# Kernel tuning notes

Measured on AMD Instinct MI355X. Metric: run time of the kernel, lower is better.

Reference implementation:

```python
import jax, jax.numpy as jnp
import numpy as np

EPS = 1e-5

def setup_inputs() -> dict:
    key = jax.random.key(0)
    k1, k2, k3, k4, k5 = jax.random.split(key, 5)
    B, C, H, W = 4, 256, 256, 256  # W == C == input_features (LayerNorm over last dim)
    O = 256  # output_features
    x = jax.random.normal(k1, (B, C, H, W), dtype=jnp.float32)
    y = jax.random.normal(k2, (B, C, H, W), dtype=jnp.float32)
    ln_weight = jax.random.normal(k3, (W,), dtype=jnp.float32) * 0.02 + 1.0
    ln_bias = jax.random.normal(k4, (W,), dtype=jnp.float32) * 0.02
    conv_weight = jax.random.normal(k5, (O, C), dtype=jnp.float32) * (1.0 / np.sqrt(C))  # 1x1 conv, no bias
    return {"x": x, "y": y, "ln_weight": ln_weight, "ln_bias": ln_bias, "conv_weight": conv_weight}


def reference(x, y, ln_weight, ln_bias, conv_weight):
    # residual add
    out = x + y  # [B, C, H, W]
    # LayerNorm over the last dim (W), matching nn.LayerNorm(normalized_shape=input_features)
    mean = jnp.mean(out, axis=-1, keepdims=True)
    var = jnp.mean(jnp.square(out - mean), axis=-1, keepdims=True)
    normed = (out - mean) * jax.lax.rsqrt(var + EPS) * ln_weight + ln_bias
    # 1x1 Conv2d (per-pixel matmul over channels), bias=False
    conv = jnp.einsum("bchw,oc->bohw", normed, conv_weight)
    # ReLU
    return jnp.maximum(conv, 0.0)
```

## Files before the change

### kernel.cpp

```cpp
#include <hip/hip_runtime.h>

typedef __bf16 bf16x8 __attribute__((ext_vector_type(8)));
typedef float floatx4 __attribute__((ext_vector_type(4)));

__device__ __forceinline__ unsigned short f2bf(float f) {
    unsigned int u = __builtin_bit_cast(unsigned int, f);
    u += 0x7fffu + ((u >> 16) & 1u);
    return (unsigned short)(u >> 16);
}

__global__ __launch_bounds__(256) void prep_kernel(const float* __restrict__ cw,
                                                   unsigned short* __restrict__ cwb,
                                                   float* __restrict__ S) {
    int o = blockIdx.x;
    int c = threadIdx.x;
    float w = cw[o * 256 + c];
    cwb[o * 256 + c] = f2bf(w);
    float s = w;
    #pragma unroll
    for (int off = 32; off; off >>= 1) s += __shfl_xor(s, off);
    __shared__ float ps[4];
    if ((c & 63) == 0) ps[c >> 6] = s;
    __syncthreads();
    if (c == 0) S[o] = ps[0] + ps[1] + ps[2] + ps[3];
}

__global__ __launch_bounds__(256) void ln_kernel(const float* __restrict__ x,
                                                 const float* __restrict__ y,
                                                 const float* __restrict__ lnw,
                                                 unsigned short* __restrict__ zhat) {
    int wave = threadIdx.x >> 6;
    int lane = threadIdx.x & 63;
    size_t row = (size_t)blockIdx.x * 4 + wave;
    const float4* xp = (const float4*)(x + row * 256) + lane;
    const float4* yp = (const float4*)(y + row * 256) + lane;
    float4 xv = *xp;
    float4 yv = *yp;
    float z0 = xv.x + yv.x, z1 = xv.y + yv.y, z2 = xv.z + yv.z, z3 = xv.w + yv.w;
    float s = z0 + z1 + z2 + z3;
    float q = z0 * z0 + z1 * z1 + z2 * z2 + z3 * z3;
    #pragma unroll
    for (int off = 32; off; off >>= 1) {
        s += __shfl_xor(s, off);
        q += __shfl_xor(q, off);
    }
    float mean = s * (1.0f / 256.0f);
    float var = q * (1.0f / 256.0f) - mean * mean;
    float rstd = rsqrtf(var + 1e-5f);
    float4 w4 = *((const float4*)lnw + lane);
    ushort4 ov;
    ov.x = f2bf((z0 - mean) * rstd * w4.x);
    ov.y = f2bf((z1 - mean) * rstd * w4.y);
    ov.z = f2bf((z2 - mean) * rstd * w4.z);
    ov.w = f2bf((z3 - mean) * rstd * w4.w);
    *((ushort4*)(zhat + row * 256) + lane) = ov;
}

__global__ __launch_bounds__(256) void gemm_kernel(const unsigned short* __restrict__ zhat,
                                                   const unsigned short* __restrict__ cwb,
                                                   const float* __restrict__ S,
                                                   const float* __restrict__ lnb,
                                                   float* __restrict__ out) {
    constexpr int LDK = 264;
    __shared__ unsigned short bt[64 * LDK];

    int id = blockIdx.x;
    int b = id >> 10;
    int tile = id & 1023;
    int p0 = tile * 64;
    const unsigned short* zb = zhat + ((size_t)b << 24) + p0;
    int t = threadIdx.x;

    {
        int c0 = t >> 3;
        int n0 = (t & 7) * 8;
        #pragma unroll
        for (int pass = 0; pass < 8; ++pass) {
            int c = c0 + pass * 32;
            uint4 v = *(const uint4*)(zb + (size_t)c * 65536 + n0);
            unsigned int vv[4] = {v.x, v.y, v.z, v.w};
            #pragma unroll
            for (int q = 0; q < 4; ++q) {
                bt[(n0 + 2 * q + 0) * LDK + c] = (unsigned short)(vv[q] & 0xffffu);
                bt[(n0 + 2 * q + 1) * LDK + c] = (unsigned short)(vv[q] >> 16);
            }
        }
    }
    __syncthreads();

    int wave = t >> 6;
    int lane = t & 63;
    int llo = lane & 15;
    int lhi = lane >> 4;
    int o_base = wave * 64;

    floatx4 acc[4][4];
    #pragma unroll
    for (int u = 0; u < 4; ++u)
        #pragma unroll
        for (int s = 0; s < 4; ++s)
            #pragma unroll
            for (int r = 0; r < 4; ++r) acc[u][s][r] = 0.0f;

    #pragma unroll
    for (int kt = 0; kt < 8; ++kt) {
        int k0 = kt * 32;
        bf16x8 bfrag[4], afrag[4];
        #pragma unroll
        for (int s = 0; s < 4; ++s)
            bfrag[s] = *(const bf16x8*)&bt[(16 * s + llo) * LDK + k0 + lhi * 8];
        #pragma unroll
        for (int u = 0; u < 4; ++u)
            afrag[u] = *(const bf16x8*)(cwb + (size_t)(o_base + 16 * u + llo) * 256 + k0 + lhi * 8);
        #pragma unroll
        for (int u = 0; u < 4; ++u)
            #pragma unroll
            for (int s = 0; s < 4; ++s)
                acc[u][s] = __builtin_amdgcn_mfma_f32_16x16x32_bf16(afrag[u], bfrag[s], acc[u][s], 0, 0, 0);
    }

    float lnbv[4];
    #pragma unroll
    for (int s = 0; s < 4; ++s) lnbv[s] = lnb[(p0 + 16 * s + llo) & 255];
    float* outb = out + ((size_t)b << 24) + p0;
    #pragma unroll
    for (int u = 0; u < 4; ++u) {
        #pragma unroll
        for (int r = 0; r < 4; ++r) {
            int o = o_base + 16 * u + 4 * lhi + r;
            float so = S[o];
            #pragma unroll
            for (int s = 0; s < 4; ++s) {
                float v = acc[u][s][r] + so * lnbv[s];
                v = v > 0.0f ? v : 0.0f;
                outb[(size_t)o * 65536 + 16 * s + llo] = v;
            }
        }
    }
}

extern "C" void kernel_launch(void* const* d_in, const int* in_sizes, int n_in,
                              void* d_out, int out_size, void* d_ws, size_t ws_size,
                              hipStream_t stream) {
    const float* x   = (const float*)d_in[0];
    const float* y   = (const float*)d_in[1];
    const float* lnw = (const float*)d_in[2];
    const float* lnb = (const float*)d_in[3];
    const float* cw  = (const float*)d_in[4];
    float* out = (float*)d_out;

    unsigned short* zhat = (unsigned short*)d_ws;
    unsigned short* cwb  = (unsigned short*)((char*)d_ws + (size_t)134217728);
    float* S             = (float*)((char*)d_ws + (size_t)134217728 + 131072);

    prep_kernel<<<256, 256, 0, stream>>>(cw, cwb, S);
    ln_kernel<<<65536, 256, 0, stream>>>(x, y, lnw, zhat);
    gemm_kernel<<<4096, 256, 0, stream>>>(zhat, cwb, S, lnb, out);
}
```

Before: 691.2 us.

## Fuse residual LayerNorm into 1x1-conv GEMM via LDS-staged bf16 tile per row

```diff
diff --git a/kernel.cpp b/kernel.cpp
--- a/kernel.cpp
+++ b/kernel.cpp
@@ -25,115 +25,122 @@
     if (c == 0) S[o] = ps[0] + ps[1] + ps[2] + ps[3];
 }
 
-__global__ __launch_bounds__(256) void ln_kernel(const float* __restrict__ x,
-                                                 const float* __restrict__ y,
-                                                 const float* __restrict__ lnw,
-                                                 unsigned short* __restrict__ zhat) {
-    int wave = threadIdx.x >> 6;
-    int lane = threadIdx.x & 63;
-    size_t row = (size_t)blockIdx.x * 4 + wave;
-    const float4* xp = (const float4*)(x + row * 256) + lane;
-    const float4* yp = (const float4*)(y + row * 256) + lane;
-    float4 xv = *xp;
-    float4 yv = *yp;
-    float z0 = xv.x + yv.x, z1 = xv.y + yv.y, z2 = xv.z + yv.z, z3 = xv.w + yv.w;
-    float s = z0 + z1 + z2 + z3;
-    float q = z0 * z0 + z1 * z1 + z2 * z2 + z3 * z3;
+__global__ __launch_bounds__(512) void fused_kernel(const float* __restrict__ x,
+                                                    const float* __restrict__ y,
+                                                    const float* __restrict__ lnw,
+                                                    const float* __restrict__ lnb,
+                                                    const unsigned short* __restrict__ cwb,
+                                                    const float* __restrict__ S,
+                                                    float* __restrict__ out) {
+    __shared__ unsigned short zt[256 * 256];
+
+    int b = blockIdx.x >> 8;
+    int h = blockIdx.x & 255;
+    int t = threadIdx.x;
+    int wave = t >> 6;
+    int lane = t & 63;
+    size_t plane = ((size_t)b << 24) + ((size_t)h << 8);
+
+    float lw[4];
     #pragma unroll
-    for (int off = 32; off; off >>= 1) {
-        s += __shfl_xor(s, off);
-        q += __shfl_xor(q, off);
-    }
-    float mean = s * (1.0f / 256.0f);
-    float var = q * (1.0f / 256.0f) - mean * mean;
-    float rstd = rsqrtf(var + 1e-5f);
-    float4 w4 = *((const float4*)lnw + lane);
-    ushort4 ov;
-    ov.x = f2bf((z0 - mean) * rstd * w4.x);
-    ov.y = f2bf((z1 - mean) * rstd * w4.y);
-    ov.z = f2bf((z2 - mean) * rstd * w4.z);
-    ov.w = f2bf((z3 - mean) * rstd * w4.w);
-    *((ushort4*)(zhat + row * 256) + lane) = ov;
-}
+    for (int j = 0; j < 4; ++j) lw[j] = lnw[lane + 64 * j];
 
-__global__ __launch_bounds__(256) void gemm_kernel(const unsigned short* __restrict__ zhat,
-                                                   const unsigned short* __restrict__ cwb,
-                                                   const float* __restrict__ S,
-                                                   const float* __restrict__ lnb,
-                                                   float* __restrict__ out) {
-    constexpr int LDK = 264;
-    __shared__ unsigned short bt[64 * LDK];
-
-    int id = blockIdx.x;
-    int b = id >> 10;
-    int tile = id & 1023;
-    int p0 = tile * 64;
-    const unsigned short* zb = zhat + ((size_t)b << 24) + p0;
-    int t = threadIdx.x;
-
-    {
-        int c0 = t >> 3;
-        int n0 = (t & 7) * 8;
+    #pragma unroll
+    for (int g = 0; g < 4; ++g) {
+        int c0 = wave * 32 + g * 8;
+        unsigned short fr[4][8];
         #pragma unroll
-        for (int pass = 0; pass < 8; ++pass) {
-            int c = c0 + pass * 32;
-            uint4 v = *(const uint4*)(zb + (size_t)c * 65536 + n0);
-            unsigned int vv[4] = {v.x, v.y, v.z, v.w};
+        for (int r = 0; r < 8; ++r) {
+            int c = c0 + r;
+            const float* xp = x + plane + ((size_t)c << 16);
+            const float* yp = y + plane + ((size_t)c << 16);
+            float z[4];
+            float s = 0.0f, q = 0.0f;
             #pragma unroll
-            for (int q = 0; q < 4; ++q) {
-                bt[(n0 + 2 * q + 0) * LDK + c] = (unsigned short)(vv[q] & 0xffffu);
-                bt[(n0 + 2 * q + 1) * LDK + c] = (unsigned short)(vv[q] >> 16);
+            for (int j = 0; j < 4; ++j) {
+                float xv = xp[lane + 64 * j];
+                float yv = yp[lane + 64 * j];
+                z[j] = xv + yv;
+                s += z[j];
+                q += z[j] * z[j];
             }
+            #pragma unroll
+            for (int off = 32; off; off >>= 1) {
+                s += __shfl_xor(s, off);
+                q += __shfl_xor(q, off);
+            }
+            float mean = s * (1.0f / 256.0f);
+            float rstd = rsqrtf(q * (1.0f / 256.0f) - mean * mean + 1e-5f);
+            #pragma unroll
+            for (int j = 0; j < 4; ++j) fr[j][r] = f2bf((z[j] - mean) * rstd * lw[j]);
+        }
+        int chunk = c0 >> 3;
+        int chunkp = chunk ^ (lane & 7);
+        #pragma unroll
+        for (int j = 0; j < 4; ++j) {
+            int w = lane + 64 * j;
+            uint4 v;
+            v.x = (unsigned int)fr[j][0] | ((unsigned int)fr[j][1] << 16);
+            v.y = (unsigned int)fr[j][2] | ((unsigned int)fr[j][3] << 16);
+            v.z = (unsigned int)fr[j][4] | ((unsigned int)fr[j][5] << 16);
+            v.w = (unsigned int)fr[j][6] | ((unsigned int)fr[j][7] << 16);
+            *(uint4*)&zt[w * 256 + chunkp * 8] = v;
         }
     }
     __syncthreads();
 
-    int wave = t >> 6;
-    int lane = t & 63;
     int llo = lane & 15;
     int lhi = lane >> 4;
-    int o_base = wave * 64;
-
-    floatx4 acc[4][4];
-    #pragma unroll
-    for (int u = 0; u < 4; ++u)
-        #pragma unroll
-        for (int s = 0; s < 4; ++s)
-            #pragma unroll
-            for (int r = 0; r < 4; ++r) acc[u][s][r] = 0.0f;
+    int o_base = (wave & 3) * 64;
+    int ptbase = (wave >> 2) * 2;
+    float* ob = out + plane;
 
     #pragma unroll
-    for (int kt = 0; kt < 8; ++kt) {
-        int k0 = kt * 32;
-        bf16x8 bfrag[4], afrag[4];
-        #pragma unroll
-        for (int s = 0; s < 4; ++s)
-            bfrag[s] = *(const bf16x8*)&bt[(16 * s + llo) * LDK + k0 + lhi * 8];
-        #pragma unroll
-        for (int u = 0; u < 4; ++u)
-            afrag[u] = *(const bf16x8*)(cwb + (size_t)(o_base + 16 * u + llo) * 256 + k0 + lhi * 8);
+    for (int pi = 0; pi < 2; ++pi) {
+        int p0 = (ptbase + pi) * 64;
+
+        floatx4 acc[4][4];
         #pragma unroll
         for (int u = 0; u < 4; ++u)
             #pragma unroll
-            for (int s = 0; s < 4; ++s)
-                acc[u][s] = __builtin_amdgcn_mfma_f32_16x16x32_bf16(afrag[u], bfrag[s], acc[u][s], 0, 0, 0);
-    }
+            for (int s2 = 0; s2 < 4; ++s2)
+                #pragma unroll
+                for (int r = 0; r < 4; ++r) acc[u][s2][r] = 0.0f;
 
-    float lnbv[4];
-    #pragma unroll
-    for (int s = 0; s < 4; ++s) lnbv[s] = lnb[(p0 + 16 * s + llo) & 255];
-    float* outb = out + ((size_t)b << 24) + p0;
-    #pragma unroll
-    for (int u = 0; u < 4; ++u) {
         #pragma unroll
-        for (int r = 0; r < 4; ++r) {
-            int o = o_base + 16 * u + 4 * lhi + r;
-            float so = S[o];
+        for (int kt = 0; kt < 8; ++kt) {
+            bf16x8 bfrag[4], afrag[4];
             #pragma unroll
-            for (int s = 0; s < 4; ++s) {
-                float v = acc[u][s][r] + so * lnbv[s];
-                v = v > 0.0f ? v : 0.0f;
-                outb[(size_t)o * 65536 + 16 * s + llo] = v;
+            for (int s2 = 0; s2 < 4; ++s2) {
+                int w = p0 + 16 * s2 + llo;
+                int chunkp = (kt * 4 + lhi) ^ (llo & 7);
+                bfrag[s2] = *(const bf16x8*)&zt[w * 256 + chunkp * 8];
+            }
+            #pragma unroll
+            for (int u = 0; u < 4; ++u)
+                afrag[u] = *(const bf16x8*)(cwb + (size_t)(o_base + 16 * u + llo) * 256 + kt * 32 + lhi * 8);
+            #pragma unroll
+            for (int u = 0; u < 4; ++u)
+                #pragma unroll
+                for (int s2 = 0; s2 < 4; ++s2)
+                    acc[u][s2] = __builtin_amdgcn_mfma_f32_16x16x32_bf16(afrag[u], bfrag[s2], acc[u][s2], 0, 0, 0);
+        }
+
+        float lnbv[4];
+        #pragma unroll
+        for (int s2 = 0; s2 < 4; ++s2) lnbv[s2] = lnb[p0 + 16 * s2 + llo];
+        #pragma unroll
+        for (int u = 0; u < 4; ++u) {
+            #pragma unroll
+            for (int r = 0; r < 4; ++r) {
+                int o = o_base + 16 * u + 4 * lhi + r;
+                float so = S[o];
+                #pragma unroll
+                for (int s2 = 0; s2 < 4; ++s2) {
+                    float v = acc[u][s2][r] + so * lnbv[s2];
+                    v = v > 0.0f ? v : 0.0f;
+                    ob[((size_t)o << 16) + p0 + 16 * s2 + llo] = v;
+                }
             }
         }
     }
@@ -149,11 +156,9 @@
     const float* cw  = (const float*)d_in[4];
     float* out = (float*)d_out;
 
-    unsigned short* zhat = (unsigned short*)d_ws;
-    unsigned short* cwb  = (unsigned short*)((char*)d_ws + (size_t)134217728);
-    float* S             = (float*)((char*)d_ws + (size_t)134217728 + 131072);
+    unsigned short* cwb = (unsigned short*)d_ws;
+    float* S            = (float*)((char*)d_ws + 131072);
 
     prep_kernel<<<256, 256, 0, stream>>>(cw, cwb, S);
-    ln_kernel<<<65536, 256, 0, stream>>>(x, y, lnw, zhat);
-    gemm_kernel<<<4096, 256, 0, stream>>>(zhat, cwb, S, lnb, out);
+    fused_kernel<<<1024, 512, 0, stream>>>(x, y, lnw, lnb, cwb, S, out);
 }
```

After: 639.0 us. -7.6%, faster.
